# Kernel tuning notes

Measured on AMD Instinct MI355X. Metric: run time of the kernel, lower is better.

The kernel has to match this reference:

```python
import jax, jax.numpy as jnp
from jax import lax
import numpy as np
import math

B_SZ, SEQ, D_MODEL = 2, 2048, 2048
D_INNER, D_STATE, D_CONV, HEADS, P, CHUNK = 4096, 128, 4, 64, 64, 128
CONV_DIM = D_INNER + 2 * D_STATE
D_IN_PROJ = 2 * D_INNER + 2 * D_STATE + HEADS


def setup_inputs() -> dict:
    key = jax.random.key(0)
    ks = jax.random.split(key, 6)
    hidden_states = jax.random.normal(ks[0], (B_SZ, SEQ, D_MODEL), jnp.float32)
    W_in = jax.random.normal(ks[1], (D_IN_PROJ, D_MODEL), jnp.float32) * 0.02
    W_conv = jax.random.normal(ks[2], (CONV_DIM, 1, D_CONV), jnp.float32) * 0.2
    b_conv = jnp.zeros((CONV_DIM,), jnp.float32)
    A_log = jnp.log(jnp.arange(1, HEADS + 1, dtype=jnp.float32))
    D = jnp.ones((HEADS,), jnp.float32)
    # dt_bias init as in the torch module
    dt = jnp.exp(jax.random.uniform(ks[3], (HEADS,)) * (math.log(0.1) - math.log(0.001)) + math.log(0.001))
    dt = jnp.clip(dt, 1e-4, None)
    dt_bias = dt + jnp.log(-jnp.expm1(-dt))
    norm_weight = jnp.ones((D_INNER,), jnp.float32)
    W_out = jax.random.normal(ks[4], (D_MODEL, D_INNER), jnp.float32) * 0.02
    return {"hidden_states": hidden_states, "W_in": W_in, "W_conv": W_conv, "b_conv": b_conv,
            "A_log": A_log, "D": D, "dt_bias": dt_bias, "norm_weight": norm_weight, "W_out": W_out}


def _mamba2_core(hidden_states, W_in, W_conv, b_conv, A_log, D, dt_bias, norm_weight, W_out):
    Bsz, L, _ = hidden_states.shape
    NC = L // CHUNK
    zxbcdt = hidden_states @ W_in.T                         # [B,L,d_in_proj]
    z = zxbcdt[..., :D_INNER]
    xBC = zxbcdt[..., D_INNER:D_INNER + CONV_DIM]
    dt = zxbcdt[..., -HEADS:]
    # causal depthwise conv1d over sequence
    xc = jnp.swapaxes(xBC, 1, 2)                            # [B,C,L]
    xc = lax.conv_general_dilated(xc, W_conv, (1,), [(D_CONV - 1, 0)],
                                  feature_group_count=CONV_DIM,
                                  dimension_numbers=('NCH', 'OIH', 'NCH'))
    xc = xc + b_conv[None, :, None]
    xBC = jax.nn.silu(jnp.swapaxes(xc, 1, 2))               # [B,L,conv_dim]
    x = xBC[..., :D_INNER]
    Bm = xBC[..., D_INNER:D_INNER + D_STATE]                # num_groups=1
    Cm = xBC[..., -D_STATE:]
    dt = jax.nn.softplus(dt + dt_bias)                      # [B,L,H]; dt_limit (0,inf) is a no-op
    A = -jnp.exp(A_log)                                     # [H]
    # --- chunked SSD scan (chunk_size = CHUNK), same math as torch_ssm ---
    xch = x.reshape(Bsz, NC, CHUNK, HEADS, P)
    dtc = dt.reshape(Bsz, NC, CHUNK, HEADS)
    Bc = Bm.reshape(Bsz, NC, CHUNK, D_STATE)
    Cc = Cm.reshape(Bsz, NC, CHUNK, D_STATE)
    u = xch * dtc[..., None]                                # [b,c,l,h,p]
    dA = dtc * A                                            # [b,c,l,h]
    dA_cs = jnp.cumsum(dA, axis=2)                          # [b,c,l,h]
    # within-chunk causal attention-like term
    seg = dA_cs[:, :, :, None, :] - dA_cs[:, :, None, :, :] # [b,c,l,s,h]
    mask = jnp.tril(jnp.ones((CHUNK, CHUNK), bool))
    Lmat = jnp.exp(jnp.where(mask[None, None, :, :, None], seg, -jnp.inf))
    CB = jnp.einsum('bcln,bcsn->bcls', Cc, Bc)
    M = CB[..., None] * Lmat                                # [b,c,l,s,h]
    Y_diag = jnp.einsum('bclsh,bcshp->bclhp', M, u)
    # per-chunk final states
    decay_states = jnp.exp(dA_cs[:, :, -1:, :] - dA_cs)     # [b,c,l,h]
    states = jnp.einsum('bcln,bclh,bclhp->bchpn', Bc, decay_states, u)
    chunk_decay = jnp.exp(dA_cs[:, :, -1, :])               # [b,c,h]
    # inter-chunk recurrence over NC chunks
    def step(h, inp):
        st, cd = inp                                        # [b,h,p,n], [b,h]
        h_new = h * cd[:, :, None, None] + st
        return h_new, h                                     # emit state at chunk start
    sts = jnp.moveaxis(states, 1, 0)
    cds = jnp.moveaxis(chunk_decay, 1, 0)
    h0 = jnp.zeros((Bsz, HEADS, P, D_STATE), hidden_states.dtype)
    _, h_starts = lax.scan(step, h0, (sts, cds))
    h_starts = jnp.moveaxis(h_starts, 0, 1)                 # [b,c,h,p,n]
    state_decay_out = jnp.exp(dA_cs)                        # [b,c,l,h]
    Y_off = jnp.einsum('bcln,bclh,bchpn->bclhp', Cc, state_decay_out, h_starts)
    Y = Y_diag + Y_off + D[None, None, None, :, None] * xch
    y = Y.reshape(Bsz, L, D_INNER)
    # gated RMSNorm (gate first, then norm; group_size == d_inner)
    yg = y * jax.nn.silu(z)
    var = jnp.mean(yg * yg, axis=-1, keepdims=True)
    y = yg * lax.rsqrt(var + 1e-5) * norm_weight
    return y @ W_out.T


def reference(hidden_states, W_in, W_conv, b_conv, A_log, D, dt_bias, norm_weight, W_out):
    return _mamba2_core(hidden_states, W_in, W_conv, b_conv, A_log, D, dt_bias, norm_weight, W_out)
```

## Files before the change

### kernel.cpp

```cpp
#include <hip/hip_runtime.h>
#include <hip/hip_bf16.h>
#include <stdint.h>

typedef __bf16 bf16;
typedef __bf16 bf16x8 __attribute__((ext_vector_type(8)));
typedef __bf16 bf16x4 __attribute__((ext_vector_type(4)));
typedef float f32x4v __attribute__((ext_vector_type(4)));

#define SEQ    2048
#define DMODEL 2048
#define DI     4096
#define NH     64
#define PDIM   64
#define CHUNKL 128
#define NCH    16
#define CONVD  4352
#define DPROJ  8512
#define ZLD    8704
#define NTOK   4096
#define LP     136

__device__ __forceinline__ float sigmoid_f(float x){ return 1.f/(1.f+expf(-x)); }
__device__ __forceinline__ float silu_f(float x){ return x*sigmoid_f(x); }
__device__ __forceinline__ float softplus_f(float x){ return x > 20.f ? x : log1pf(expf(x)); }

__global__ __launch_bounds__(256) void cvt_f32_bf16(const float* __restrict__ src,
                                                    bf16* __restrict__ dst, int n){
    int i = (blockIdx.x*256 + threadIdx.x)*4;
    if (i + 3 >= n) return;
    float4 v = *(const float4*)&src[i];
    bf16x4 o; o[0]=(bf16)v.x; o[1]=(bf16)v.y; o[2]=(bf16)v.z; o[3]=(bf16)v.w;
    *(bf16x4*)&dst[i] = o;
}

__global__ __launch_bounds__(256) void cvt_pad_rows(const float* __restrict__ src,
                                                    bf16* __restrict__ dst,
                                                    int rows_valid, int total){
    int i = (blockIdx.x*256 + threadIdx.x)*4;
    if (i + 3 >= total) return;
    int r = i >> 11;
    bf16x4 o;
    if (r < rows_valid){
        float4 v = *(const float4*)&src[i];
        o[0]=(bf16)v.x; o[1]=(bf16)v.y; o[2]=(bf16)v.z; o[3]=(bf16)v.w;
    } else {
        o[0]=(bf16)0.f; o[1]=(bf16)0.f; o[2]=(bf16)0.f; o[3]=(bf16)0.f;
    }
    *(bf16x4*)&dst[i] = o;
}

#define READ_A(BUFP, QM)                                                               \
    {                                                                                  \
        _Pragma("unroll")                                                              \
        for (int i=0;i<4;i++)                                                          \
            _Pragma("unroll")                                                          \
            for (int k2=0;k2<2;k2++)                                                   \
                af[i][k2] = *(const bf16x8*)&(BUFP)[aoff[i][k2] + (QM)*8192];          \
    }

#define READ_B(BUFP, QN)                                                               \
    {                                                                                  \
        _Pragma("unroll")                                                              \
        for (int nf=0;nf<2;nf++)                                                       \
            _Pragma("unroll")                                                          \
            for (int k2=0;k2<2;k2++)                                                   \
                bfr[nf][k2] = *(const bf16x8*)&(BUFP)[boff[nf][k2] + (QN)*8192];       \
    }

#define MMA_Q(QM, QN)                                                                  \
    {                                                                                  \
        __builtin_amdgcn_s_setprio(1);                                                 \
        _Pragma("unroll")                                                              \
        for (int i=0;i<4;i++)                                                          \
            _Pragma("unroll")                                                          \
            for (int nf=0;nf<2;nf++)                                                   \
                _Pragma("unroll")                                                      \
                for (int k2=0;k2<2;k2++)                                               \
                    acc[(QM)*4+i][(QN)*2+nf] = __builtin_amdgcn_mfma_f32_16x16x32_bf16( \
                        af[i][k2], bfr[nf][k2], acc[(QM)*4+i][(QN)*2+nf], 0,0,0);      \
        __builtin_amdgcn_s_setprio(0);                                                 \
    }

#define SBAR() do { __builtin_amdgcn_sched_barrier(0);                                 \
                    __builtin_amdgcn_s_barrier();                                      \
                    asm volatile("s_waitcnt lgkmcnt(0)" ::: "memory");                 \
                    __builtin_amdgcn_sched_barrier(0); } while(0)
#define EBAR() do { __builtin_amdgcn_s_barrier();                                      \
                    __builtin_amdgcn_sched_barrier(0); } while(0)

template<int MODE>
__global__ __launch_bounds__(512) void gemm256_kernel(const bf16* __restrict__ A,
                                                      const bf16* __restrict__ Bmat,
                                                      void* __restrict__ Cout,
                                                      int NXB, int NYB, int K, int ldc){
    __shared__ __align__(16) bf16 lds[2][2*16384];
    const int tid  = threadIdx.x;
    const int w    = tid >> 6;
    const int lane = tid & 63;
    const int wm   = w >> 2, wn = w & 3;

    int bid = blockIdx.x;
    int x, y, kz = 0;
    if (MODE == 3){
        kz = bid >> 5;
        int t32 = bid & 31;
        x = 32 + (t32 & 1);
        y = t32 >> 1;
    } else {
        int nb2  = (MODE==2) ? ((int)gridDim.x >> 1) : (int)gridDim.x;
        if (MODE == 2){ kz = bid / nb2; bid = bid % nb2; }
        int wg   = (bid & 7)*(nb2 >> 3) + (bid >> 3);
        const int SW = 8;
        int sup = wg / (SW*NYB);
        int rr  = wg % (SW*NYB);
        int x0  = sup*SW;
        int wl  = (NXB - x0 < SW) ? (NXB - x0) : SW;
        x = x0 + rr % wl;
        y = rr / wl;
    }
    const int tm = y*256, tn = x*256;

    const int KT  = (MODE==3) ? 8 : ((MODE==2) ? (K >> 7) : (K >> 6));
    const int kt0 = kz * KT;

    f32x4v acc[8][4];
    #pragma unroll
    for (int i=0;i<8;i++)
        #pragma unroll
        for (int j=0;j<4;j++) acc[i][j] = {0.f,0.f,0.f,0.f};
    bf16x8 af[4][2];
    bf16x8 bfr[2][2];

    const bf16* srcA[2][2];
    const bf16* srcB[2][2];
    #pragma unroll
    for (int r0h=0;r0h<2;r0h++)
        #pragma unroll
        for (int i=0;i<2;i++){
            int lr = r0h*128 + i*64 + (tid>>3);
            int growA = tm + ((lr>>6)&1)*128 + (lr>>7)*64 + (lr&63);
            int growB = tn + ((lr>>5)&3)*64 + (lr>>7)*32 + (lr&31);
            int gslot = (tid&7) ^ (lr&7);
            srcA[r0h][i] = A + (long)growA*K + gslot*8;
            srcB[r0h][i] = Bmat + (long)growB*K + gslot*8;
        }
    int aoff[4][2], boff[2][2];
    #pragma unroll
    for (int i=0;i<4;i++)
        #pragma unroll
        for (int k2=0;k2<2;k2++){
            int ra0 = wm*64 + i*16 + (lane&15);
            int slot = (k2*4 + (lane>>4)) ^ (ra0&7);
            aoff[i][k2] = ra0*64 + slot*8;
        }
    #pragma unroll
    for (int nf=0;nf<2;nf++)
        #pragma unroll
        for (int k2=0;k2<2;k2++){
            int rb0 = wn*32 + nf*16 + (lane&15);
            int slot = (k2*4 + (lane>>4)) ^ (rb0&7);
            boff[nf][k2] = 16384 + rb0*64 + slot*8;
        }

    auto stageA = [&](int buf, int t, int r0h){
        long koff = (long)(kt0 + t)*64;
        #pragma unroll
        for (int i=0;i<2;i++){
            bf16* dst = &lds[buf][0] + (size_t)(r0h*128 + i*64 + w*8)*64;
            __builtin_amdgcn_global_load_lds(
                (const __attribute__((address_space(1))) void*)(srcA[r0h][i] + koff),
                (__attribute__((address_space(3))) void*)dst, 16, 0, 0);
        }
    };
    auto stageB = [&](int buf, int t, int r0h){
        long koff = (long)(kt0 + t)*64;
        #pragma unroll
        for (int i=0;i<2;i++){
            bf16* dst = &lds[buf][16384] + (size_t)(r0h*128 + i*64 + w*8)*64;
            __builtin_amdgcn_global_load_lds(
                (const __attribute__((address_space(1))) void*)(srcB[r0h][i] + koff),
                (__attribute__((address_space(3))) void*)dst, 16, 0, 0);
        }
    };

    stageA(0, 0, 0);
    stageB(0, 0, 0);
    stageA(0, 0, 1);
    stageB(0, 0, 1);
    if (KT > 1){ stageA(1, 1, 0); stageB(1, 1, 0); }
    asm volatile("s_waitcnt vmcnt(8)" ::: "memory");
    __builtin_amdgcn_s_barrier();

    int cur = 0;
    for (int t = 0; t < KT; ++t){
        int nxt = cur ^ 1;
        const bf16* bufc = &lds[cur][0];
        READ_A(bufc, 0)
        READ_B(bufc, 0)
        if (t+1 < KT) stageA(nxt, t+1, 1);
        asm volatile("s_waitcnt vmcnt(6)" ::: "memory");
        SBAR();
        MMA_Q(0, 0)
        READ_B(bufc, 1)
        if (t+1 < KT) stageB(nxt, t+1, 1);
        SBAR();
        MMA_Q(0, 1)
        READ_A(bufc, 1)
        READ_B(bufc, 0)
        if (t+2 < KT) stageA(cur, t+2, 0);
        SBAR();
        MMA_Q(1, 0)
        EBAR();
        READ_B(bufc, 1)
        if (t+2 < KT) stageB(cur, t+2, 0);
        asm volatile("s_waitcnt vmcnt(8)" ::: "memory");
        SBAR();
        MMA_Q(1, 1)
        cur = nxt;
    }

    const int er = (lane>>4)*4, ec = lane&15;
    #pragma unroll
    for (int mi=0;mi<8;mi++)
        #pragma unroll
        for (int ni=0;ni<4;ni++){
            long r0 = tm + wm*128 + mi*16 + er;
            int  c0 = tn + wn*64 + ni*16 + ec;
            #pragma unroll
            for (int j=0;j<4;j++){
                float val = acc[mi][ni][j];
                if (MODE == 1){
                    ((bf16*)Cout)[(r0+j)*ldc + c0] = (bf16)val;
                } else if (MODE == 2){
                    ((float*)Cout)[(long)kz*NYB*256*ldc + (r0+j)*ldc + c0] = val;
                } else {
                    ((float*)Cout)[((long)kz*4096 + (r0+j))*512 + (c0 - 8192)] = val;
                }
            }
        }
}

__global__ __launch_bounds__(256) void tailreduce_kernel(const float* __restrict__ p,
                                                         bf16* __restrict__ zx,
                                                         float* __restrict__ dtf){
    long i = ((long)blockIdx.x*256 + threadIdx.x)*4;
    int r = (int)(i >> 9);
    int c = (int)(i & 511);
    const long Q = (long)4096*512;
    float4 a  = *(const float4*)&p[i];
    float4 b  = *(const float4*)&p[i+Q];
    float4 cc = *(const float4*)&p[i+2*Q];
    float4 d  = *(const float4*)&p[i+3*Q];
    float s0 = a.x+b.x+cc.x+d.x, s1 = a.y+b.y+cc.y+d.y;
    float s2 = a.z+b.z+cc.z+d.z, s3 = a.w+b.w+cc.w+d.w;
    bf16x4 o; o[0]=(bf16)s0; o[1]=(bf16)s1; o[2]=(bf16)s2; o[3]=(bf16)s3;
    *(bf16x4*)&zx[(long)r*ZLD + 8192 + c] = o;
    int col = 8192 + c;
    float sv[4] = {s0,s1,s2,s3};
    #pragma unroll
    for (int j=0;j<4;j++){
        int cj = col + j;
        if (cj >= 8448 && cj < 8512) dtf[(long)r*64 + (cj-8448)] = sv[j];
    }
}

__global__ __launch_bounds__(256) void reduce_add_kernel(const float* __restrict__ p,
                                                         float* __restrict__ out, int n){
    int i = (blockIdx.x*256 + threadIdx.x)*4;
    if (i + 3 >= n) return;
    float4 a = *(const float4*)&p[i];
    float4 b = *(const float4*)&p[i + 8388608];
    a.x+=b.x; a.y+=b.y; a.z+=b.z; a.w+=b.w;
    *(float4*)&out[i] = a;
}

__global__ __launch_bounds__(256) void conv_silu_kernel(const bf16* __restrict__ zx,
                                                        const float* __restrict__ Wc,
                                                        const float* __restrict__ bc,
                                                        bf16* __restrict__ xc){
    int ch  = blockIdx.x*256 + threadIdx.x;
    int byy = blockIdx.y;
    int b = byy >> 8, t0 = (byy & 255)*8;
    float w0=Wc[ch*4+0], w1=Wc[ch*4+1], w2=Wc[ch*4+2], w3=Wc[ch*4+3];
    float bcv = bc[ch];
    const bf16* col = zx + (long)(b*SEQ)*ZLD + 4096 + ch;
    float v[11];
    #pragma unroll
    for (int k=0;k<11;k++){
        int t = t0 - 3 + k;
        v[k] = (t >= 0) ? (float)col[(long)t*ZLD] : 0.f;
    }
    bf16* orow = xc + (long)(b*SEQ + t0)*CONVD + ch;
    #pragma unroll
    for (int j=0;j<8;j++){
        float acc = bcv + v[j]*w0 + v[j+1]*w1 + v[j+2]*w2 + v[j+3]*w3;
        orow[(long)j*CONVD] = (bf16)silu_f(acc);
    }
}

__global__ __launch_bounds__(256) void dtcum_kernel(const float* __restrict__ dtf,
                                                    const float* __restrict__ A_log,
                                                    const float* __restrict__ dt_bias,
                                                    float* __restrict__ dtv,
                                                    float* __restrict__ dacs,
                                                    float* __restrict__ cdec){
    int wid  = (blockIdx.x*256 + threadIdx.x) >> 6;
    int lane = threadIdx.x & 63;
    int h  = wid & 63, bc = wid >> 6;
    int b  = bc >> 4,  c  = bc & 15;
    float Ah   = -expf(A_log[h]);
    float bias = dt_bias[h];
    long tok0 = (long)(b*SEQ + c*CHUNKL);
    int l0 = lane*2;
    float d0 = softplus_f(dtf[(tok0+l0)*64 + h] + bias);
    float d1 = softplus_f(dtf[(tok0+l0+1)*64 + h] + bias);
    float s = (d0 + d1)*Ah;
    #pragma unroll
    for (int off=1; off<64; off<<=1){
        float t = __shfl_up(s, off, 64);
        if (lane >= off) s += t;
    }
    long base_h = (long)wid*128;
    float cs1 = s;
    float cs0 = s - d1*Ah;
    dtv[base_h+l0]   = d0;  dtv[base_h+l0+1]  = d1;
    dacs[base_h+l0]  = cs0; dacs[base_h+l0+1] = cs1;
    if (lane == 63) cdec[wid] = expf(cs1);
}

__global__ __launch_bounds__(256) void cb_mfma_kernel(const bf16* __restrict__ xc,
                                                      float* __restrict__ cb){
    __shared__ __align__(16) bf16 A1[128*LP];
    __shared__ __align__(16) bf16 B1[128*LP];
    int blk = blockIdx.x;  int b = blk>>4, c = blk&15;
    int tid = threadIdx.x;
    const int w = tid >> 6, lane = tid & 63;
    long tok0 = (long)(b*SEQ + c*CHUNKL);
    int l = tid>>1, n0 = (tid&1)*64;
    const bf16* crow = xc + tok0*CONVD + (long)l*CONVD;
    #pragma unroll
    for (int v=0;v<8;v++){
        *(bf16x8*)&A1[l*LP + n0 + v*8] = *(const bf16x8*)&crow[4224 + n0 + v*8];
        *(bf16x8*)&B1[l*LP + n0 + v*8] = *(const bf16x8*)&crow[4096 + n0 + v*8];
    }
    __syncthreads();
    f32x4v acc[2][8];
    #pragma unroll
    for (int mi=0;mi<2;mi++)
        #pragma unroll
        for (int ni=0;ni<8;ni++) acc[mi][ni] = {0.f,0.f,0.f,0.f};
    #pragma unroll
    for (int kk=0; kk<128; kk+=32){
        bf16x8 afr[2], bfr2[8];
        #pragma unroll
        for (int mi=0;mi<2;mi++)
            afr[mi] = *(const bf16x8*)&A1[(w*32 + mi*16 + (lane&15))*LP + kk + (lane>>4)*8];
        #pragma unroll
        for (int ni=0;ni<8;ni++)
            bfr2[ni] = *(const bf16x8*)&B1[(ni*16 + (lane&15))*LP + kk + (lane>>4)*8];
        #pragma unroll
        for (int mi=0;mi<2;mi++)
            #pragma unroll
            for (int ni=0;ni<8;ni++)
                acc[mi][ni] = __builtin_amdgcn_mfma_f32_16x16x32_bf16(afr[mi], bfr2[ni], acc[mi][ni], 0,0,0);
    }
    float* out = cb + (long)blk*16384;
    #pragma unroll
    for (int mi=0;mi<2;mi++)
        #pragma unroll
        for (int ni=0;ni<8;ni++){
            int r0 = w*32 + mi*16 + (lane>>4)*4;
            int c0 = ni*16 + (lane&15);
            #pragma unroll
            for (int j=0;j<4;j++) out[(long)(r0+j)*128 + c0] = acc[mi][ni][j];
        }
}

__global__ __launch_bounds__(256) void states_mfma_kernel(const bf16* __restrict__ xc,
                                                          const float* __restrict__ dtv,
                                                          const float* __restrict__ dacs,
                                                          bf16* __restrict__ states){
    __shared__ __align__(16) bf16 A1[64*LP];
    __shared__ __align__(16) bf16 B1[128*LP];
    __shared__ float wgtl[128];
    int blk = blockIdx.x;
    int h = blk & 63, bc = blk >> 6;
    int b = bc >> 4, c = bc & 15;
    int tid = threadIdx.x;
    const int w = tid >> 6, lane = tid & 63;
    long tok0 = (long)(b*SEQ + c*CHUNKL);
    long base_h = (long)blk*128;
    float cs_last = dacs[base_h + 127];
    if (tid < 128) wgtl[tid] = dtv[base_h+tid] * expf(cs_last - dacs[base_h+tid]);
    __syncthreads();
    #pragma unroll
    for (int t=0;t<4;t++){
        int l = (tid>>3) + t*32;
        int p0 = (tid&7)*8;
        bf16x8 xv = *(const bf16x8*)&xc[(tok0+l)*CONVD + h*64 + p0];
        float wv = wgtl[l];
        #pragma unroll
        for (int e=0;e<8;e++) A1[(p0+e)*LP + l] = (bf16)((float)xv[e]*wv);
    }
    {
        int l = tid>>1, n0 = (tid&1)*64;
        const bf16* brow = xc + (tok0+l)*CONVD + 4096;
        #pragma unroll
        for (int v=0;v<8;v++){
            bf16x8 bv = *(const bf16x8*)&brow[n0 + v*8];
            #pragma unroll
            for (int e=0;e<8;e++) B1[(n0+v*8+e)*LP + l] = bv[e];
        }
    }
    __syncthreads();
    f32x4v acc[8];
    #pragma unroll
    for (int ni=0;ni<8;ni++) acc[ni] = {0.f,0.f,0.f,0.f};
    #pragma unroll
    for (int kk=0; kk<128; kk+=32){
        bf16x8 afr = *(const bf16x8*)&A1[(w*16 + (lane&15))*LP + kk + (lane>>4)*8];
        #pragma unroll
        for (int ni=0;ni<8;ni++){
            bf16x8 bfr2 = *(const bf16x8*)&B1[(ni*16 + (lane&15))*LP + kk + (lane>>4)*8];
            acc[ni] = __builtin_amdgcn_mfma_f32_16x16x32_bf16(afr, bfr2, acc[ni], 0,0,0);
        }
    }
    bf16* out = states + (long)blk*8192;
    #pragma unroll
    for (int ni=0;ni<8;ni++){
        int p0 = w*16 + (lane>>4)*4;
        int n  = ni*16 + (lane&15);
        #pragma unroll
        for (int j=0;j<4;j++) out[(long)(p0+j)*128 + n] = (bf16)acc[ni][j];
    }
}

__global__ __launch_bounds__(256) void scan_kernel(const bf16* __restrict__ states,
                                                   const float* __restrict__ cdec,
                                                   bf16* __restrict__ hst){
    long gid = (long)blockIdx.x*256 + threadIdx.x;
    int n = gid & 127;
    int p = (gid >> 7) & 63;
    int h = (gid >> 13) & 63;
    int b = (int)(gid >> 19);
    float hrun = 0.f;
    for (int c=0;c<16;c++){
        long idx = ((((long)(b*16 + c)*64 + h)*64 + p)*128) + n;
        hst[idx] = (bf16)hrun;
        hrun = hrun * cdec[(b*16+c)*64 + h] + (float)states[idx];
    }
}

__global__ __launch_bounds__(256) void yfused_kernel(const bf16* __restrict__ xc,
                                                     const float* __restrict__ cb,
                                                     const bf16* __restrict__ hst,
                                                     const float* __restrict__ dtv,
                                                     const float* __restrict__ dacs,
                                                     bf16* __restrict__ Ybf){
    __shared__ __align__(16) bf16 A1[128*LP];
    __shared__ __align__(16) bf16 B1[64*LP];
    __shared__ float csl[128];
    int blk = blockIdx.x;
    int h = blk & 63, bc = blk >> 6;
    int b = bc >> 4, c = bc & 15;
    int tid = threadIdx.x;
    const int w = tid >> 6, lane = tid & 63;
    long tok0 = (long)(b*SEQ + c*CHUNKL);
    long base_h = (long)blk*128;
    if (tid < 128) csl[tid] = dacs[base_h + tid];
    __syncthreads();
    {
        int l = tid>>1, s0 = (tid&1)*64;
        float el = csl[l];
        const float* cbrow = cb + (long)bc*16384 + (long)l*128 + s0;
        #pragma unroll 8
        for (int j=0;j<64;j++){
            int s = s0 + j;
            float v = (s <= l) ? cbrow[j]*expf(el - csl[s]) : 0.f;
            A1[l*LP + s] = (bf16)v;
        }
    }
    #pragma unroll
    for (int t=0;t<4;t++){
        int s = (tid>>3) + t*32;
        int p0 = (tid&7)*8;
        bf16x8 xv = *(const bf16x8*)&xc[(tok0+s)*CONVD + h*64 + p0];
        float wv = dtv[base_h + s];
        #pragma unroll
        for (int e=0;e<8;e++) B1[(p0+e)*LP + s] = (bf16)((float)xv[e]*wv);
    }
    __syncthreads();
    f32x4v acc[2][4];
    #pragma unroll
    for (int mi=0;mi<2;mi++)
        #pragma unroll
        for (int ni=0;ni<4;ni++) acc[mi][ni] = {0.f,0.f,0.f,0.f};
    #pragma unroll
    for (int kk=0; kk<128; kk+=32){
        bf16x8 afr[2], bfr2[4];
        #pragma unroll
        for (int mi=0;mi<2;mi++)
            afr[mi] = *(const bf16x8*)&A1[(w*32 + mi*16 + (lane&15))*LP + kk + (lane>>4)*8];
        #pragma unroll
        for (int ni=0;ni<4;ni++)
            bfr2[ni] = *(const bf16x8*)&B1[(ni*16 + (lane&15))*LP + kk + (lane>>4)*8];
        #pragma unroll
        for (int mi=0;mi<2;mi++)
            #pragma unroll
            for (int ni=0;ni<4;ni++)
                acc[mi][ni] = __builtin_amdgcn_mfma_f32_16x16x32_bf16(afr[mi], bfr2[ni], acc[mi][ni], 0,0,0);
    }
    __syncthreads();
    {
        int l = tid>>1, n0 = (tid&1)*64;
        float e1 = expf(csl[l]);
        const bf16* crow = xc + (tok0+l)*CONVD + 4224;
        #pragma unroll
        for (int v=0;v<8;v++){
            bf16x8 cv = *(const bf16x8*)&crow[n0 + v*8];
            bf16x8 o;
            #pragma unroll
            for (int e=0;e<8;e++) o[e] = (bf16)((float)cv[e]*e1);
            *(bf16x8*)&A1[l*LP + n0 + v*8] = o;
        }
    }
    {
        int p = tid>>2, n0 = (tid&3)*32;
        const bf16* hrow = hst + (long)blk*8192 + (long)p*128 + n0;
        #pragma unroll
        for (int v=0;v<4;v++)
            *(bf16x8*)&B1[p*LP + n0 + v*8] = *(const bf16x8*)&hrow[v*8];
    }
    __syncthreads();
    #pragma unroll
    for (int kk=0; kk<128; kk+=32){
        bf16x8 afr[2], bfr2[4];
        #pragma unroll
        for (int mi=0;mi<2;mi++)
            afr[mi] = *(const bf16x8*)&A1[(w*32 + mi*16 + (lane&15))*LP + kk + (lane>>4)*8];
        #pragma unroll
        for (int ni=0;ni<4;ni++)
            bfr2[ni] = *(const bf16x8*)&B1[(ni*16 + (lane&15))*LP + kk + (lane>>4)*8];
        #pragma unroll
        for (int mi=0;mi<2;mi++)
            #pragma unroll
            for (int ni=0;ni<4;ni++)
                acc[mi][ni] = __builtin_amdgcn_mfma_f32_16x16x32_bf16(afr[mi], bfr2[ni], acc[mi][ni], 0,0,0);
    }
    #pragma unroll
    for (int mi=0;mi<2;mi++)
        #pragma unroll
        for (int ni=0;ni<4;ni++){
            int l0 = w*32 + mi*16 + (lane>>4)*4;
            int p  = ni*16 + (lane&15);
            #pragma unroll
            for (int j=0;j<4;j++)
                Ybf[(tok0 + l0 + j)*DI + h*64 + p] = (bf16)acc[mi][ni][j];
        }
}

__global__ __launch_bounds__(256) void gatenorm_kernel(const bf16* __restrict__ Ybf,
                                                       const bf16* __restrict__ zx,
                                                       const bf16* __restrict__ xc,
                                                       const float* __restrict__ Dp,
                                                       const float* __restrict__ nw,
                                                       bf16* __restrict__ ybn){
    __shared__ float red[4];
    int tok = blockIdx.x, tid = threadIdx.x;
    const bf16* yrow = Ybf + (long)tok*DI;
    const bf16* zrow = zx  + (long)tok*ZLD;
    const bf16* xrow = xc  + (long)tok*CONVD;
    float yg[16];
    float ss = 0.f;
    #pragma unroll
    for (int k=0;k<4;k++){
        int d = (tid + k*256)*4;
        bf16x4 yv = *(const bf16x4*)&yrow[d];
        bf16x4 zv = *(const bf16x4*)&zrow[d];
        bf16x4 xv = *(const bf16x4*)&xrow[d];
        float dh = Dp[d>>6];
        #pragma unroll
        for (int e=0;e<4;e++){
            float yy = (float)yv[e] + dh*(float)xv[e];
            float g = yy*silu_f((float)zv[e]);
            yg[k*4+e] = g;
            ss += g*g;
        }
    }
    #pragma unroll
    for (int off=32; off>0; off>>=1) ss += __shfl_down(ss, off, 64);
    if ((tid & 63) == 0) red[tid>>6] = ss;
    __syncthreads();
    float tot = red[0]+red[1]+red[2]+red[3];
    float scale = rsqrtf(tot/(float)DI + 1e-5f);
    #pragma unroll
    for (int k=0;k<4;k++){
        int d = (tid + k*256)*4;
        float4 wv = *(const float4*)&nw[d];
        bf16x4 o;
        o[0]=(bf16)(yg[k*4+0]*scale*wv.x);
        o[1]=(bf16)(yg[k*4+1]*scale*wv.y);
        o[2]=(bf16)(yg[k*4+2]*scale*wv.z);
        o[3]=(bf16)(yg[k*4+3]*scale*wv.w);
        *(bf16x4*)&ybn[(long)tok*DI + d] = o;
    }
}

extern "C" void kernel_launch(void* const* d_in, const int* in_sizes, int n_in,
                              void* d_out, int out_size, void* d_ws, size_t ws_size,
                              hipStream_t stream){
    const float* hs      = (const float*)d_in[0];
    const float* W_in    = (const float*)d_in[1];
    const float* W_conv  = (const float*)d_in[2];
    const float* b_conv  = (const float*)d_in[3];
    const float* A_log   = (const float*)d_in[4];
    const float* Dp      = (const float*)d_in[5];
    const float* dt_bias = (const float*)d_in[6];
    const float* nw      = (const float*)d_in[7];
    const float* W_out   = (const float*)d_in[8];
    float* out = (float*)d_out;

    char* ws = (char*)d_ws;
    const size_t OFF_ZX    = 0;
    const size_t OFF_DTF   = 71303168;
    const size_t OFF_XC    = 72351744;
    const size_t OFF_DTV   = 108003328;
    const size_t OFF_DACS  = 109051904;
    const size_t OFF_CDEC  = 110100480;
    const size_t OFF_CB    = 110108672;
    const size_t OFF_SLOTA = 112205824;
    const size_t OFF_SLOTB = 179314688;
    const size_t OFF_WOUTB = 212869120;

    bf16*  zx    = (bf16*)(ws + OFF_ZX);
    float* dtf   = (float*)(ws + OFF_DTF);
    bf16*  xc    = (bf16*)(ws + OFF_XC);
    float* dtv   = (float*)(ws + OFF_DTV);
    float* dacs  = (float*)(ws + OFF_DACS);
    float* cdec  = (float*)(ws + OFF_CDEC);
    float* cbuf  = (float*)(ws + OFF_CB);
    bf16*  hsb   = (bf16*)(ws + OFF_SLOTA);
    bf16*  winb  = (bf16*)(ws + OFF_SLOTA + 16777216);
    bf16*  states= (bf16*)(ws + OFF_SLOTA);
    bf16*  Ybf   = (bf16*)(ws + OFF_SLOTA);
    float* part  = (float*)(ws + OFF_SLOTA);
    float* tpart = (float*)(ws + OFF_SLOTB);
    bf16*  hst   = (bf16*)(ws + OFF_SLOTB);
    bf16*  ybn   = (bf16*)(ws + OFF_SLOTB);
    bf16*  woutb = (bf16*)(ws + OFF_WOUTB);

    cvt_f32_bf16<<<8192, 256, 0, stream>>>(hs, hsb, NTOK*DMODEL);
    cvt_pad_rows<<<17408, 256, 0, stream>>>(W_in, winb, DPROJ, ZLD*DMODEL);
    cvt_f32_bf16<<<8192, 256, 0, stream>>>(W_out, woutb, DMODEL*DI);

    gemm256_kernel<1><<<512, 512, 0, stream>>>(hsb, winb, (void*)zx,
                                               32, 16, DMODEL, ZLD);
    gemm256_kernel<3><<<128, 512, 0, stream>>>(hsb, winb, (void*)tpart,
                                               34, 16, DMODEL, ZLD);
    tailreduce_kernel<<<2048, 256, 0, stream>>>(tpart, zx, dtf);

    conv_silu_kernel<<<dim3(17, 512), 256, 0, stream>>>(zx, W_conv, b_conv, xc);
    dtcum_kernel<<<512, 256, 0, stream>>>(dtf, A_log, dt_bias, dtv, dacs, cdec);
    cb_mfma_kernel<<<32, 256, 0, stream>>>(xc, cbuf);
    states_mfma_kernel<<<2048, 256, 0, stream>>>(xc, dtv, dacs, states);
    scan_kernel<<<4096, 256, 0, stream>>>(states, cdec, hst);
    yfused_kernel<<<2048, 256, 0, stream>>>(xc, cbuf, hst, dtv, dacs, Ybf);
    gatenorm_kernel<<<4096, 256, 0, stream>>>(Ybf, zx, xc, Dp, nw, ybn);

    gemm256_kernel<2><<<256, 512, 0, stream>>>(ybn, woutb, (void*)part,
                                               8, 16, DI, DMODEL);
    reduce_add_kernel<<<8192, 256, 0, stream>>>(part, out, NTOK*DMODEL);
}
```

Baseline: 444.7 us.

## Replace split-K out-projection with 256x128 tile GEMM, fuse conversions, vectorize conv and norm

The output projection no longer uses a split-K GEMM that writes fp32 partials and then runs a separate reduce kernel. A new 256x128-tile GEMM with a triple-buffered LDS pipeline writes the final output directly, which removes the partial-buffer traffic and one launch. The three fp32-to-bf16 conversion kernels are merged into a single launch. The conv+SiLU kernel now handles four channels per thread with vector loads, and the gated-norm kernel moves to 8-wide bf16 accesses. The big GEMM also gets tighter vmcnt waits on its last iterations.

```diff
diff --git a/kernel.cpp b/kernel.cpp
--- a/kernel.cpp
+++ b/kernel.cpp
@@ -24,29 +24,35 @@
 __device__ __forceinline__ float silu_f(float x){ return x*sigmoid_f(x); }
 __device__ __forceinline__ float softplus_f(float x){ return x > 20.f ? x : log1pf(expf(x)); }
 
-__global__ __launch_bounds__(256) void cvt_f32_bf16(const float* __restrict__ src,
-                                                    bf16* __restrict__ dst, int n){
-    int i = (blockIdx.x*256 + threadIdx.x)*4;
-    if (i + 3 >= n) return;
-    float4 v = *(const float4*)&src[i];
-    bf16x4 o; o[0]=(bf16)v.x; o[1]=(bf16)v.y; o[2]=(bf16)v.z; o[3]=(bf16)v.w;
-    *(bf16x4*)&dst[i] = o;
-}
-
-__global__ __launch_bounds__(256) void cvt_pad_rows(const float* __restrict__ src,
-                                                    bf16* __restrict__ dst,
-                                                    int rows_valid, int total){
-    int i = (blockIdx.x*256 + threadIdx.x)*4;
-    if (i + 3 >= total) return;
-    int r = i >> 11;
-    bf16x4 o;
-    if (r < rows_valid){
-        float4 v = *(const float4*)&src[i];
-        o[0]=(bf16)v.x; o[1]=(bf16)v.y; o[2]=(bf16)v.z; o[3]=(bf16)v.w;
+__global__ __launch_bounds__(256) void cvt_all_kernel(const float* __restrict__ hs,
+                                                      const float* __restrict__ W_in,
+                                                      const float* __restrict__ W_out,
+                                                      bf16* __restrict__ hsb,
+                                                      bf16* __restrict__ winb,
+                                                      bf16* __restrict__ woutb){
+    int blk = blockIdx.x;
+    if (blk < 8192){
+        int i = (blk*256 + threadIdx.x)*4;
+        float4 v = *(const float4*)&hs[i];
+        bf16x4 o; o[0]=(bf16)v.x; o[1]=(bf16)v.y; o[2]=(bf16)v.z; o[3]=(bf16)v.w;
+        *(bf16x4*)&hsb[i] = o;
+    } else if (blk < 25600){
+        int i = ((blk-8192)*256 + threadIdx.x)*4;
+        int r = i >> 11;
+        bf16x4 o;
+        if (r < DPROJ){
+            float4 v = *(const float4*)&W_in[i];
+            o[0]=(bf16)v.x; o[1]=(bf16)v.y; o[2]=(bf16)v.z; o[3]=(bf16)v.w;
+        } else {
+            o[0]=(bf16)0.f; o[1]=(bf16)0.f; o[2]=(bf16)0.f; o[3]=(bf16)0.f;
+        }
+        *(bf16x4*)&winb[i] = o;
     } else {
-        o[0]=(bf16)0.f; o[1]=(bf16)0.f; o[2]=(bf16)0.f; o[3]=(bf16)0.f;
-    }
-    *(bf16x4*)&dst[i] = o;
+        int i = ((blk-25600)*256 + threadIdx.x)*4;
+        float4 v = *(const float4*)&W_out[i];
+        bf16x4 o; o[0]=(bf16)v.x; o[1]=(bf16)v.y; o[2]=(bf16)v.z; o[3]=(bf16)v.w;
+        *(bf16x4*)&woutb[i] = o;
+    }
 }
 
 #define READ_A(BUFP, QM)                                                               \
@@ -107,8 +113,7 @@
         x = 32 + (t32 & 1);
         y = t32 >> 1;
     } else {
-        int nb2  = (MODE==2) ? ((int)gridDim.x >> 1) : (int)gridDim.x;
-        if (MODE == 2){ kz = bid / nb2; bid = bid % nb2; }
+        int nb2  = (int)gridDim.x;
         int wg   = (bid & 7)*(nb2 >> 3) + (bid >> 3);
         const int SW = 8;
         int sup = wg / (SW*NYB);
@@ -120,7 +125,7 @@
     }
     const int tm = y*256, tn = x*256;
 
-    const int KT  = (MODE==3) ? 8 : ((MODE==2) ? (K >> 7) : (K >> 6));
+    const int KT  = (MODE==3) ? 8 : (K >> 6);
     const int kt0 = kz * KT;
 
     f32x4v acc[8][4];
@@ -197,8 +202,12 @@
         const bf16* bufc = &lds[cur][0];
         READ_A(bufc, 0)
         READ_B(bufc, 0)
-        if (t+1 < KT) stageA(nxt, t+1, 1);
-        asm volatile("s_waitcnt vmcnt(6)" ::: "memory");
+        if (t+1 < KT){
+            stageA(nxt, t+1, 1);
+            asm volatile("s_waitcnt vmcnt(6)" ::: "memory");
+        } else {
+            asm volatile("s_waitcnt vmcnt(0)" ::: "memory");
+        }
         SBAR();
         MMA_Q(0, 0)
         READ_B(bufc, 1)
@@ -212,8 +221,12 @@
         MMA_Q(1, 0)
         EBAR();
         READ_B(bufc, 1)
-        if (t+2 < KT) stageB(cur, t+2, 0);
-        asm volatile("s_waitcnt vmcnt(8)" ::: "memory");
+        if (t+2 < KT){
+            stageB(cur, t+2, 0);
+            asm volatile("s_waitcnt vmcnt(8)" ::: "memory");
+        } else {
+            asm volatile("s_waitcnt vmcnt(4)" ::: "memory");
+        }
         SBAR();
         MMA_Q(1, 1)
         cur = nxt;
@@ -231,12 +244,136 @@
                 float val = acc[mi][ni][j];
                 if (MODE == 1){
                     ((bf16*)Cout)[(r0+j)*ldc + c0] = (bf16)val;
-                } else if (MODE == 2){
-                    ((float*)Cout)[(long)kz*NYB*256*ldc + (r0+j)*ldc + c0] = val;
                 } else {
                     ((float*)Cout)[((long)kz*4096 + (r0+j))*512 + (c0 - 8192)] = val;
                 }
             }
+        }
+}
+
+__global__ __launch_bounds__(512) void gemm256x128_kernel(const bf16* __restrict__ A,
+                                                          const bf16* __restrict__ Bmat,
+                                                          float* __restrict__ C,
+                                                          int NXB, int NYB, int K, int ldc){
+    __shared__ __align__(16) bf16 lds[3][24576];
+    const int tid  = threadIdx.x;
+    const int w    = tid >> 6;
+    const int lane = tid & 63;
+    const int wm   = w >> 2, wn = w & 3;
+
+    int bid = blockIdx.x, nb = gridDim.x;
+    int wg = (bid & 7)*(nb >> 3) + (bid >> 3);
+    const int SW = 8;
+    int sup = wg / (SW*NYB);
+    int rr  = wg % (SW*NYB);
+    int x0  = sup*SW;
+    int wl  = (NXB - x0 < SW) ? (NXB - x0) : SW;
+    int x   = x0 + rr % wl;
+    int y   = rr / wl;
+    const int tm = y*256, tn = x*128;
+    const int KT = K >> 6;
+
+    f32x4v acc[8][2];
+    #pragma unroll
+    for (int i=0;i<8;i++)
+        #pragma unroll
+        for (int j=0;j<2;j++) acc[i][j] = {0.f,0.f,0.f,0.f};
+    bf16x8 af[4][2];
+    bf16x8 bfr[2][2];
+
+    const bf16* srcA[2][2];
+    const bf16* srcB[2];
+    #pragma unroll
+    for (int r0h=0;r0h<2;r0h++)
+        #pragma unroll
+        for (int i=0;i<2;i++){
+            int lr = r0h*128 + i*64 + (tid>>3);
+            int growA = tm + ((lr>>6)&1)*128 + (lr>>7)*64 + (lr&63);
+            int gslot = (tid&7) ^ (lr&7);
+            srcA[r0h][i] = A + (long)growA*K + gslot*8;
+        }
+    #pragma unroll
+    for (int i=0;i<2;i++){
+        int lr = i*64 + (tid>>3);
+        int growB = tn + lr;
+        int gslot = (tid&7) ^ (lr&7);
+        srcB[i] = Bmat + (long)growB*K + gslot*8;
+    }
+    int aoff[4][2], boff[2][2];
+    #pragma unroll
+    for (int i=0;i<4;i++)
+        #pragma unroll
+        for (int k2=0;k2<2;k2++){
+            int ra0 = wm*64 + i*16 + (lane&15);
+            int slot = (k2*4 + (lane>>4)) ^ (ra0&7);
+            aoff[i][k2] = ra0*64 + slot*8;
+        }
+    #pragma unroll
+    for (int nf=0;nf<2;nf++)
+        #pragma unroll
+        for (int k2=0;k2<2;k2++){
+            int rb0 = wn*32 + nf*16 + (lane&15);
+            int slot = (k2*4 + (lane>>4)) ^ (rb0&7);
+            boff[nf][k2] = 16384 + rb0*64 + slot*8;
+        }
+
+    auto stageA = [&](int buf, int t, int r0h){
+        long koff = (long)t*64;
+        #pragma unroll
+        for (int i=0;i<2;i++){
+            bf16* dst = &lds[buf][0] + (size_t)(r0h*128 + i*64 + w*8)*64;
+            __builtin_amdgcn_global_load_lds(
+                (const __attribute__((address_space(1))) void*)(srcA[r0h][i] + koff),
+                (__attribute__((address_space(3))) void*)dst, 16, 0, 0);
+        }
+    };
+    auto stageB = [&](int buf, int t){
+        long koff = (long)t*64;
+        #pragma unroll
+        for (int i=0;i<2;i++){
+            bf16* dst = &lds[buf][16384] + (size_t)(i*64 + w*8)*64;
+            __builtin_amdgcn_global_load_lds(
+                (const __attribute__((address_space(1))) void*)(srcB[i] + koff),
+                (__attribute__((address_space(3))) void*)dst, 16, 0, 0);
+        }
+    };
+
+    stageA(0, 0, 0); stageA(0, 0, 1); stageB(0, 0);
+    if (KT > 1){ stageA(1, 1, 0); stageA(1, 1, 1); stageB(1, 1); }
+    asm volatile("s_waitcnt vmcnt(6)" ::: "memory");
+    __builtin_amdgcn_s_barrier();
+
+    int cur = 0;
+    for (int t = 0; t < KT; ++t){
+        int stb = cur + 2; if (stb >= 3) stb -= 3;
+        const bf16* bufc = &lds[cur][0];
+        READ_A(bufc, 0)
+        READ_B(bufc, 0)
+        if (t+2 < KT){ stageA(stb, t+2, 0); stageA(stb, t+2, 1); }
+        SBAR();
+        MMA_Q(0, 0)
+        READ_A(bufc, 1)
+        if (t+2 < KT){
+            stageB(stb, t+2);
+            asm volatile("s_waitcnt vmcnt(6)" ::: "memory");
+        } else {
+            asm volatile("s_waitcnt vmcnt(0)" ::: "memory");
+        }
+        SBAR();
+        MMA_Q(1, 0)
+        cur = (cur == 2) ? 0 : cur + 1;
+    }
+
+    const int er = (lane>>4)*4, ec = lane&15;
+    #pragma unroll
+    for (int mi=0;mi<8;mi++)
+        #pragma unroll
+        for (int ni=0;ni<2;ni++){
+            long r0 = tm + wm*128 + mi*16 + er;
+            int  c0 = tn + wn*32 + ni*16 + ec;
+            #pragma unroll
+            for (int j=0;j<4;j++)
+                C[(r0+j)*ldc + c0] = acc[mi][ni][j];
         }
 }
 
@@ -264,37 +401,38 @@
     }
 }
 
-__global__ __launch_bounds__(256) void reduce_add_kernel(const float* __restrict__ p,
-                                                         float* __restrict__ out, int n){
-    int i = (blockIdx.x*256 + threadIdx.x)*4;
-    if (i + 3 >= n) return;
-    float4 a = *(const float4*)&p[i];
-    float4 b = *(const float4*)&p[i + 8388608];
-    a.x+=b.x; a.y+=b.y; a.z+=b.z; a.w+=b.w;
-    *(float4*)&out[i] = a;
-}
-
 __global__ __launch_bounds__(256) void conv_silu_kernel(const bf16* __restrict__ zx,
                                                         const float* __restrict__ Wc,
                                                         const float* __restrict__ bc,
                                                         bf16* __restrict__ xc){
-    int ch  = blockIdx.x*256 + threadIdx.x;
+    int c4 = blockIdx.x*256 + threadIdx.x;
+    if (c4 >= 1088) return;
+    int ch = c4*4;
     int byy = blockIdx.y;
     int b = byy >> 8, t0 = (byy & 255)*8;
-    float w0=Wc[ch*4+0], w1=Wc[ch*4+1], w2=Wc[ch*4+2], w3=Wc[ch*4+3];
-    float bcv = bc[ch];
+    float4 tap[4];
+    #pragma unroll
+    for (int e=0;e<4;e++) tap[e] = *(const float4*)&Wc[(ch+e)*4];
+    float4 bq = *(const float4*)&bc[ch];
+    float bca[4] = {bq.x, bq.y, bq.z, bq.w};
     const bf16* col = zx + (long)(b*SEQ)*ZLD + 4096 + ch;
-    float v[11];
+    bf16x4 v[11];
     #pragma unroll
     for (int k=0;k<11;k++){
         int t = t0 - 3 + k;
-        v[k] = (t >= 0) ? (float)col[(long)t*ZLD] : 0.f;
-    }
-    bf16* orow = xc + (long)(b*SEQ + t0)*CONVD + ch;
+        if (t >= 0) v[k] = *(const bf16x4*)&col[(long)t*ZLD];
+        else { v[k][0]=(bf16)0.f; v[k][1]=(bf16)0.f; v[k][2]=(bf16)0.f; v[k][3]=(bf16)0.f; }
+    }
     #pragma unroll
     for (int j=0;j<8;j++){
-        float acc = bcv + v[j]*w0 + v[j+1]*w1 + v[j+2]*w2 + v[j+3]*w3;
-        orow[(long)j*CONVD] = (bf16)silu_f(acc);
+        bf16x4 o;
+        #pragma unroll
+        for (int e=0;e<4;e++){
+            float acc = bca[e] + (float)v[j][e]*tap[e].x + (float)v[j+1][e]*tap[e].y
+                               + (float)v[j+2][e]*tap[e].z + (float)v[j+3][e]*tap[e].w;
+            o[e] = (bf16)silu_f(acc);
+        }
+        *(bf16x4*)&xc[(long)(b*SEQ + t0 + j)*CONVD + ch] = o;
     }
 }
 
@@ -573,17 +711,17 @@
     float yg[16];
     float ss = 0.f;
     #pragma unroll
-    for (int k=0;k<4;k++){
-        int d = (tid + k*256)*4;
-        bf16x4 yv = *(const bf16x4*)&yrow[d];
-        bf16x4 zv = *(const bf16x4*)&zrow[d];
-        bf16x4 xv = *(const bf16x4*)&xrow[d];
+    for (int k=0;k<2;k++){
+        int d = (tid + k*256)*8;
+        bf16x8 yv = *(const bf16x8*)&yrow[d];
+        bf16x8 zv = *(const bf16x8*)&zrow[d];
+        bf16x8 xv = *(const bf16x8*)&xrow[d];
         float dh = Dp[d>>6];
         #pragma unroll
-        for (int e=0;e<4;e++){
+        for (int e=0;e<8;e++){
             float yy = (float)yv[e] + dh*(float)xv[e];
             float g = yy*silu_f((float)zv[e]);
-            yg[k*4+e] = g;
+            yg[k*8+e] = g;
             ss += g*g;
         }
     }
@@ -594,15 +732,15 @@
     float tot = red[0]+red[1]+red[2]+red[3];
     float scale = rsqrtf(tot/(float)DI + 1e-5f);
     #pragma unroll
-    for (int k=0;k<4;k++){
-        int d = (tid + k*256)*4;
-        float4 wv = *(const float4*)&nw[d];
-        bf16x4 o;
-        o[0]=(bf16)(yg[k*4+0]*scale*wv.x);
-        o[1]=(bf16)(yg[k*4+1]*scale*wv.y);
-        o[2]=(bf16)(yg[k*4+2]*scale*wv.z);
-        o[3]=(bf16)(yg[k*4+3]*scale*wv.w);
-        *(bf16x4*)&ybn[(long)tok*DI + d] = o;
+    for (int k=0;k<2;k++){
+        int d = (tid + k*256)*8;
+        float4 w0 = *(const float4*)&nw[d];
+        float4 w1 = *(const float4*)&nw[d+4];
+        float wv[8] = {w0.x,w0.y,w0.z,w0.w,w1.x,w1.y,w1.z,w1.w};
+        bf16x8 o;
+        #pragma unroll
+        for (int e=0;e<8;e++) o[e] = (bf16)(yg[k*8+e]*scale*wv[e]);
+        *(bf16x8*)&ybn[(long)tok*DI + d] = o;
     }
 }
 
@@ -643,15 +781,12 @@
     bf16*  winb  = (bf16*)(ws + OFF_SLOTA + 16777216);
     bf16*  states= (bf16*)(ws + OFF_SLOTA);
     bf16*  Ybf   = (bf16*)(ws + OFF_SLOTA);
-    float* part  = (float*)(ws + OFF_SLOTA);
     float* tpart = (float*)(ws + OFF_SLOTB);
     bf16*  hst   = (bf16*)(ws + OFF_SLOTB);
     bf16*  ybn   = (bf16*)(ws + OFF_SLOTB);
     bf16*  woutb = (bf16*)(ws + OFF_WOUTB);
 
-    cvt_f32_bf16<<<8192, 256, 0, stream>>>(hs, hsb, NTOK*DMODEL);
-    cvt_pad_rows<<<17408, 256, 0, stream>>>(W_in, winb, DPROJ, ZLD*DMODEL);
-    cvt_f32_bf16<<<8192, 256, 0, stream>>>(W_out, woutb, DMODEL*DI);
+    cvt_all_kernel<<<33792, 256, 0, stream>>>(hs, W_in, W_out, hsb, winb, woutb);
 
     gemm256_kernel<1><<<512, 512, 0, stream>>>(hsb, winb, (void*)zx,
                                                32, 16, DMODEL, ZLD);
@@ -659,7 +794,7 @@
                                                34, 16, DMODEL, ZLD);
     tailreduce_kernel<<<2048, 256, 0, stream>>>(tpart, zx, dtf);
 
-    conv_silu_kernel<<<dim3(17, 512), 256, 0, stream>>>(zx, W_conv, b_conv, xc);
+    conv_silu_kernel<<<dim3(5, 512), 256, 0, stream>>>(zx, W_conv, b_conv, xc);
     dtcum_kernel<<<512, 256, 0, stream>>>(dtf, A_log, dt_bias, dtv, dacs, cdec);
     cb_mfma_kernel<<<32, 256, 0, stream>>>(xc, cbuf);
     states_mfma_kernel<<<2048, 256, 0, stream>>>(xc, dtv, dacs, states);
@@ -667,7 +802,5 @@
     yfused_kernel<<<2048, 256, 0, stream>>>(xc, cbuf, hst, dtv, dacs, Ybf);
     gatenorm_kernel<<<4096, 256, 0, stream>>>(Ybf, zx, xc, Dp, nw, ybn);
 
-    gemm256_kernel<2><<<256, 512, 0, stream>>>(ybn, woutb, (void*)part,
-                                               8, 16, DI, DMODEL);
-    reduce_add_kernel<<<8192, 256, 0, stream>>>(part, out, NTOK*DMODEL);
-}
+    gemm256x128_kernel<<<256, 512, 0, stream>>>(ybn, woutb, out, 16, 16, DI, DMODEL);
+}
```

Result: no change. 438.1 us (-1.5%).
